# Kernel optimization log

Measured on AMD Instinct MI355X. Metric: run time of the kernel, lower is better.

The kernel has to match this reference:

```python
import jax, jax.numpy as jnp
import numpy as np

PROCESSING_STEPS = 3


def setup_inputs() -> dict:
    key = jax.random.key(0)
    ks = jax.random.split(key, 6)
    N, D, G = 500000, 128, 4096
    x = jax.random.normal(ks[0], (N, D), dtype=jnp.float32)
    # torch LSTM param layout: [4*hidden, input] and [4*hidden, hidden], gates i,f,g,o
    s = 1.0 / np.sqrt(D)
    W_ih = jax.random.uniform(ks[1], (4 * D, 2 * D), minval=-s, maxval=s, dtype=jnp.float32)
    W_hh = jax.random.uniform(ks[2], (4 * D, D), minval=-s, maxval=s, dtype=jnp.float32)
    b_ih = jax.random.uniform(ks[3], (4 * D,), minval=-s, maxval=s, dtype=jnp.float32)
    b_hh = jax.random.uniform(ks[4], (4 * D,), minval=-s, maxval=s, dtype=jnp.float32)
    index = jnp.sort(jax.random.randint(ks[5], (N,), 0, G, dtype=jnp.int64))
    return {"x": x, "W_ih": W_ih, "W_hh": W_hh, "b_ih": b_ih, "b_hh": b_hh,
            "index": index, "dim_size": G}


def _lstm_cell(inp, h, c, W_ih, W_hh, b_ih, b_hh):
    gates = inp @ W_ih.T + h @ W_hh.T + (b_ih + b_hh)  # [G, 4D]
    i, f, g, o = jnp.split(gates, 4, axis=-1)
    c = jax.nn.sigmoid(f) * c + jax.nn.sigmoid(i) * jnp.tanh(g)
    h = jax.nn.sigmoid(o) * jnp.tanh(c)
    return h, c


def reference(x, W_ih, W_hh, b_ih, b_hh, index, dim_size):
    N, D = x.shape
    h = jnp.zeros((dim_size, D), dtype=x.dtype)
    c = jnp.zeros((dim_size, D), dtype=x.dtype)
    q_star = jnp.zeros((dim_size, 2 * D), dtype=x.dtype)
    for _ in range(PROCESSING_STEPS):
        h, c = _lstm_cell(q_star, h, c, W_ih, W_hh, b_ih, b_hh)
        q = h  # [G, D]
        e = jnp.sum(x * q[index], axis=-1)  # [N]
        # segment softmax (numerically stable)
        m = jax.ops.segment_max(e, index, num_segments=dim_size)
        m = jnp.where(jnp.isfinite(m), m, 0.0)  # guard empty segments
        ex = jnp.exp(e - m[index])
        s = jax.ops.segment_sum(ex, index, num_segments=dim_size)
        a = ex / jnp.maximum(s, 1e-16)[index]  # [N]
        r = jax.ops.segment_sum(a[:, None] * x, index, num_segments=dim_size)  # [G, D]
        q_star = jnp.concatenate([q, r], axis=-1)
    return q_star
```

## Files before the change

kernel.cpp:

```cpp
#include <hip/hip_runtime.h>
#include <hip/hip_fp16.h>
#include <math.h>

#define D 128

typedef float f4v __attribute__((ext_vector_type(4)));

__device__ __forceinline__ float sigmoidf_(float x) { return 1.f / (1.f + __expf(-x)); }

__device__ __forceinline__ float4 pack8_to_half8(const float* xf) {
    __half2 hh[4];
    hh[0] = __floats2half2_rn(xf[0], xf[1]);
    hh[1] = __floats2half2_rn(xf[2], xf[3]);
    hh[2] = __floats2half2_rn(xf[4], xf[5]);
    hh[3] = __floats2half2_rn(xf[6], xf[7]);
    return *(float4*)hh;
}

__global__ void prep_kernel(const float* __restrict__ W_ih, const float* __restrict__ W_hh,
                            const float* __restrict__ b_ih, const float* __restrict__ b_hh,
                            const int* __restrict__ idx, int N, int G,
                            float* __restrict__ WcatT, int* __restrict__ seg_off,
                            float* __restrict__ b_sum, float* __restrict__ h1,
                            float* __restrict__ c1) {
    int b = blockIdx.x, t = threadIdx.x;
    if (b < 256) {
        int k = b;
        for (int j = t; j < 512; j += 256) {
            float v = W_ih[(size_t)j * 256 + k];
            if (k < 128) v += W_hh[(size_t)j * 128 + k];
            WcatT[(size_t)k * 512 + j] = v;
        }
    } else if (b < 273) {
        int g = (b - 256) * 256 + t;
        if (g <= G) {
            int lo = 0, hi = N;
            while (lo < hi) {
                int mid = (lo + hi) >> 1;
                if (idx[mid] < g) lo = mid + 1; else hi = mid;
            }
            seg_off[g] = lo;
        }
    } else {
        for (int i = t; i < 4 * D; i += 256) b_sum[i] = b_ih[i] + b_hh[i];
        if (t < D) {
            float bi = b_ih[t] + b_hh[t];
            float bg = b_ih[2 * D + t] + b_hh[2 * D + t];
            float bo = b_ih[3 * D + t] + b_hh[3 * D + t];
            float c = sigmoidf_(bi) * tanhf(bg);
            c1[t] = c;
            h1[t] = sigmoidf_(bo) * tanhf(c);
        }
    }
}

__device__ __forceinline__ void online8(const float (&xf0)[8], const float (&xf1)[8],
                                        const float4 q0, const float4 q1,
                                        int base, int wer, int qg,
                                        float& m, float& s, float (&acc)[8]) {
    float p0 = xf0[0] * q0.x + xf0[1] * q0.y + xf0[2] * q0.z + xf0[3] * q0.w
             + xf0[4] * q1.x + xf0[5] * q1.y + xf0[6] * q1.z + xf0[7] * q1.w;
    float p1 = xf1[0] * q0.x + xf1[1] * q0.y + xf1[2] * q0.z + xf1[3] * q0.w
             + xf1[4] * q1.x + xf1[5] * q1.y + xf1[6] * q1.z + xf1[7] * q1.w;
#pragma unroll
    for (int off = 1; off < 16; off <<= 1) {
        p0 += __shfl_xor(p0, off);
        p1 += __shfl_xor(p1, off);
    }
    float p0a = __shfl_xor(p0, 16), p0b = __shfl_xor(p0, 32), p0c = __shfl_xor(p0a, 32);
    float p1a = __shfl_xor(p1, 16), p1b = __shfl_xor(p1, 32), p1c = __shfl_xor(p1a, 32);
    float s00 = (base + qg       < wer) ? p0  : -INFINITY;
    float s01 = (base + (qg ^ 1) < wer) ? p0a : -INFINITY;
    float s02 = (base + (qg ^ 2) < wer) ? p0b : -INFINITY;
    float s03 = (base + (qg ^ 3) < wer) ? p0c : -INFINITY;
    float s10 = (base + 4 + qg       < wer) ? p1  : -INFINITY;
    float s11 = (base + 4 + (qg ^ 1) < wer) ? p1a : -INFINITY;
    float s12 = (base + 4 + (qg ^ 2) < wer) ? p1b : -INFINITY;
    float s13 = (base + 4 + (qg ^ 3) < wer) ? p1c : -INFINITY;

    float mn = fmaxf(fmaxf(fmaxf(s00, s01), fmaxf(s02, s03)),
                     fmaxf(fmaxf(s10, s11), fmaxf(s12, s13)));
    mn = fmaxf(m, mn);
    float al = __expf(m - mn);
    float w00 = __expf(s00 - mn), w01 = __expf(s01 - mn);
    float w02 = __expf(s02 - mn), w03 = __expf(s03 - mn);
    float w10 = __expf(s10 - mn), w11 = __expf(s11 - mn);
    float w12 = __expf(s12 - mn), w13 = __expf(s13 - mn);
    float sg = (w00 + w01) + (w02 + w03) + ((w10 + w11) + (w12 + w13));
    s = s * al + sg;
#pragma unroll
    for (int j = 0; j < 8; ++j)
        acc[j] = acc[j] * al + w00 * xf0[j] + w10 * xf1[j];
    m = mn;
}

__device__ __forceinline__ void attn_finish(float (&acc)[8], float s, int qg, int c,
                                            float* rdst, bool wr) {
#pragma unroll
    for (int j = 0; j < 8; ++j) {
        acc[j] += __shfl_xor(acc[j], 16);
        acc[j] += __shfl_xor(acc[j], 32);
    }
    if (wr && qg == 0) {
        float inv = 1.f / fmaxf(s, 1e-16f);
        float4 o0; o0.x = acc[0] * inv; o0.y = acc[1] * inv; o0.z = acc[2] * inv; o0.w = acc[3] * inv;
        float4 o1; o1.x = acc[4] * inv; o1.y = acc[5] * inv; o1.z = acc[6] * inv; o1.w = acc[7] * inv;
        *(float4*)&rdst[8 * c] = o0;
        *(float4*)&rdst[8 * c + 4] = o1;
    }
}

__device__ __forceinline__ void attn_f32(const float* __restrict__ x, __half* __restrict__ xh,
                                         int start, int end, int qg, int c,
                                         const float* qrow, float* rdst, bool wr) {
    float4 q0 = *(const float4*)&qrow[8 * c];
    float4 q1 = *(const float4*)&qrow[8 * c + 4];
    float m = -INFINITY, s = 0.f;
    float acc[8] = {0.f, 0.f, 0.f, 0.f, 0.f, 0.f, 0.f, 0.f};
    const f4v* x4 = (const f4v*)x;
    float4* xh4 = (float4*)xh;
    if (start < end) {
        int last = end - 1;
        for (int base = start; base < end; base += 8) {
            int r0 = min(base + qg, last);
            int r1 = min(base + 4 + qg, last);
            f4v f00 = __builtin_nontemporal_load(&x4[(size_t)r0 * 32 + 2 * c]);
            f4v f01 = __builtin_nontemporal_load(&x4[(size_t)r0 * 32 + 2 * c + 1]);
            f4v f10 = __builtin_nontemporal_load(&x4[(size_t)r1 * 32 + 2 * c]);
            f4v f11 = __builtin_nontemporal_load(&x4[(size_t)r1 * 32 + 2 * c + 1]);
            float xf0[8] = {f00.x, f00.y, f00.z, f00.w, f01.x, f01.y, f01.z, f01.w};
            float xf1[8] = {f10.x, f10.y, f10.z, f10.w, f11.x, f11.y, f11.z, f11.w};
            xh4[(size_t)r0 * 16 + c] = pack8_to_half8(xf0);
            xh4[(size_t)r1 * 16 + c] = pack8_to_half8(xf1);
            online8(xf0, xf1, q0, q1, base, end, qg, m, s, acc);
        }
    }
    attn_finish(acc, s, qg, c, rdst, wr);
}

__device__ __forceinline__ void attn_f16(const __half* __restrict__ xh,
                                         int start, int end, int qg, int c,
                                         const float* qrow, float* rdst, bool wr) {
    float4 q0 = *(const float4*)&qrow[8 * c];
    float4 q1 = *(const float4*)&qrow[8 * c + 4];
    float m = -INFINITY, s = 0.f;
    float acc[8] = {0.f, 0.f, 0.f, 0.f, 0.f, 0.f, 0.f, 0.f};
    const float4* x4 = (const float4*)xh;
    if (start < end) {
        int last = end - 1;
        for (int base = start; base < end; base += 8) {
            int r0 = min(base + qg, last);
            int r1 = min(base + 4 + qg, last);
            float4 v0 = x4[(size_t)r0 * 16 + c];
            float4 v1 = x4[(size_t)r1 * 16 + c];
            const __half2* h0 = (const __half2*)&v0;
            const __half2* h1 = (const __half2*)&v1;
            float2 a0 = __half22float2(h0[0]), a1 = __half22float2(h0[1]);
            float2 a2 = __half22float2(h0[2]), a3 = __half22float2(h0[3]);
            float2 b0 = __half22float2(h1[0]), b1 = __half22float2(h1[1]);
            float2 b2 = __half22float2(h1[2]), b3 = __half22float2(h1[3]);
            float xf0[8] = {a0.x, a0.y, a1.x, a1.y, a2.x, a2.y, a3.x, a3.y};
            float xf1[8] = {b0.x, b0.y, b1.x, b1.y, b2.x, b2.y, b3.x, b3.y};
            online8(xf0, xf1, q0, q1, base, end, qg, m, s, acc);
        }
    }
    attn_finish(acc, s, qg, c, rdst, wr);
}

__global__ __launch_bounds__(256, 4) void fused_kernel(
    const float* __restrict__ x, __half* __restrict__ xh,
    const int* __restrict__ seg_off, const float* __restrict__ WcatT,
    const float* __restrict__ b_sum, const float* __restrict__ h1,
    const float* __restrict__ c1, float* __restrict__ out, int G) {

    __shared__ float qs[4][256];
    __shared__ float cL[4][128];
    __shared__ float gl[4][512];
    __shared__ float bL[512];

    int tid = threadIdx.x;
    int w = tid >> 6, lane = tid & 63;
    int qg = lane >> 4, c = lane & 15;
    int gbase = blockIdx.x * 4;
    int g = gbase + w;
    bool valid = g < G;
    int start = 0, end = 0;
    if (valid) { start = seg_off[g]; end = seg_off[g + 1]; }

    for (int e = tid; e < 512; e += 256) bL[e] = b_sum[e];
    if (tid < 128) {
        float hv = h1[tid], cv = c1[tid];
#pragma unroll
        for (int s2 = 0; s2 < 4; ++s2) { qs[s2][tid] = hv; cL[s2][tid] = cv; }
    }
    __syncthreads();

    int j0 = w * 128 + 2 * lane;
    const float* wp = WcatT + j0;

    attn_f32(x, xh, start, end, qg, c, &qs[w][0], &qs[w][128], true);
    __syncthreads();

#pragma unroll 1
    for (int step = 0; step < 2; ++step) {
        float a0[4] = {0.f, 0.f, 0.f, 0.f};
        float a1[4] = {0.f, 0.f, 0.f, 0.f};
        for (int k = 0; k < 256; k += 4) {
            float qv[4][4];
            *(float4*)qv[0] = *(const float4*)&qs[0][k];
            *(float4*)qv[1] = *(const float4*)&qs[1][k];
            *(float4*)qv[2] = *(const float4*)&qs[2][k];
            *(float4*)qv[3] = *(const float4*)&qs[3][k];
#pragma unroll
            for (int dk = 0; dk < 4; ++dk) {
                float2 wv = *(const float2*)&wp[(size_t)(k + dk) * 512];
#pragma unroll
                for (int s2 = 0; s2 < 4; ++s2) {
                    a0[s2] = fmaf(qv[s2][dk], wv.x, a0[s2]);
                    a1[s2] = fmaf(qv[s2][dk], wv.y, a1[s2]);
                }
            }
        }
        float bx = bL[j0], by = bL[j0 + 1];
#pragma unroll
        for (int s2 = 0; s2 < 4; ++s2) {
            float2 o; o.x = a0[s2] + bx; o.y = a1[s2] + by;
            *(float2*)&gl[s2][j0] = o;
        }
        __syncthreads();

        bool final_step = (step == 1);
#pragma unroll
        for (int r2 = 0; r2 < 2; ++r2) {
            int e = tid + 256 * r2;
            int s2 = e >> 7, k = e & 127;
            float ig = gl[s2][k];
            float fg = gl[s2][128 + k];
            float gg = gl[s2][256 + k];
            float og = gl[s2][384 + k];
            float cp = cL[s2][k];
            float cc = sigmoidf_(fg) * cp + sigmoidf_(ig) * tanhf(gg);
            float hh = sigmoidf_(og) * tanhf(cc);
            cL[s2][k] = cc;
            qs[s2][k] = hh;
            if (final_step && (gbase + s2) < G)
                out[(size_t)(gbase + s2) * 256 + k] = hh;
        }
        __syncthreads();

        if (!final_step) {
            attn_f16(xh, start, end, qg, c, &qs[w][0], &qs[w][128], true);
        } else {
            float* rdst = valid ? (out + (size_t)g * 256 + 128) : (float*)&qs[w][128];
            attn_f16(xh, start, end, qg, c, &qs[w][0], rdst, valid);
        }
        __syncthreads();
    }
}

extern "C" void kernel_launch(void* const* d_in, const int* in_sizes, int n_in,
                              void* d_out, int out_size, void* d_ws, size_t ws_size,
                              hipStream_t stream) {
    const float* x      = (const float*)d_in[0];
    const float* W_ih   = (const float*)d_in[1];
    const float* W_hh   = (const float*)d_in[2];
    const float* b_ih   = (const float*)d_in[3];
    const float* b_hh   = (const float*)d_in[4];
    const int*   index  = (const int*)d_in[5];
    int N = in_sizes[5];
    int G = out_size / (2 * D);
    float* out = (float*)d_out;
    size_t totalx = (size_t)N * D;

    float* ws = (float*)d_ws;
    __half* xh    = (__half*)ws;
    float* WcatT  = ws + totalx / 2;
    float* b_sum  = WcatT + 256 * 512;
    float* h1     = b_sum + 4 * D;
    float* c1     = h1 + D;
    int* seg_off  = (int*)(c1 + D);

    prep_kernel<<<274, 256, 0, stream>>>(W_ih, W_hh, b_ih, b_hh, index, N, G,
                                         WcatT, seg_off, b_sum, h1, c1);

    int nb = (G + 3) >> 2;
    fused_kernel<<<nb, 256, 0, stream>>>(x, xh, seg_off, WcatT, b_sum, h1, c1, out, G);
}
```

Measured before the change: 467.7 us.

## Split each segment across two waves with split-K LSTM matvec and softmax merge

Doubles the block to 512 threads so each segment's attention pass is split between two wavefronts. Each wavefront computes a partial online softmax (max, sum, weighted accumulator), and the two halves are merged through shared memory. The LSTM gate matvec is split along K across the two 256-thread halves, with the partial sums and bias added in the cell update. The f16 pass also gains a one-iteration register prefetch. This is meant to add memory-level parallelism and occupancy for the bandwidth-bound x streaming, at the cost of extra shared-memory traffic, barriers and a combine step.

```diff
diff --git a/kernel.cpp b/kernel.cpp
--- a/kernel.cpp
+++ b/kernel.cpp
@@ -94,34 +94,37 @@
     m = mn;
 }
 
-__device__ __forceinline__ void attn_finish(float (&acc)[8], float s, int qg, int c,
-                                            float* rdst, bool wr) {
+__device__ __forceinline__ void attn_store(float (&acc)[8], float m, float s,
+                                           int seg, int half, int lane, int qg, int c,
+                                           float (*gp)[4][512],
+                                           float (*sm2)[2], float (*ss2)[2]) {
 #pragma unroll
     for (int j = 0; j < 8; ++j) {
         acc[j] += __shfl_xor(acc[j], 16);
         acc[j] += __shfl_xor(acc[j], 32);
     }
-    if (wr && qg == 0) {
-        float inv = 1.f / fmaxf(s, 1e-16f);
-        float4 o0; o0.x = acc[0] * inv; o0.y = acc[1] * inv; o0.z = acc[2] * inv; o0.w = acc[3] * inv;
-        float4 o1; o1.x = acc[4] * inv; o1.y = acc[5] * inv; o1.z = acc[6] * inv; o1.w = acc[7] * inv;
-        *(float4*)&rdst[8 * c] = o0;
-        *(float4*)&rdst[8 * c + 4] = o1;
-    }
-}
-
-__device__ __forceinline__ void attn_f32(const float* __restrict__ x, __half* __restrict__ xh,
-                                         int start, int end, int qg, int c,
-                                         const float* qrow, float* rdst, bool wr) {
+    if (qg == 0) {
+#pragma unroll
+        for (int j = 0; j < 8; ++j) gp[half][seg][8 * c + j] = acc[j];
+    }
+    if (lane == 0) { sm2[seg][half] = m; ss2[seg][half] = s; }
+}
+
+__device__ __forceinline__ void attn_pass_f32(const float* __restrict__ x,
+                                              __half* __restrict__ xh,
+                                              int ws, int we, int seg, int half,
+                                              int lane, int qg, int c, const float* qrow,
+                                              float (*gp)[4][512],
+                                              float (*sm2)[2], float (*ss2)[2]) {
     float4 q0 = *(const float4*)&qrow[8 * c];
     float4 q1 = *(const float4*)&qrow[8 * c + 4];
     float m = -INFINITY, s = 0.f;
     float acc[8] = {0.f, 0.f, 0.f, 0.f, 0.f, 0.f, 0.f, 0.f};
     const f4v* x4 = (const f4v*)x;
     float4* xh4 = (float4*)xh;
-    if (start < end) {
-        int last = end - 1;
-        for (int base = start; base < end; base += 8) {
+    if (ws < we) {
+        int last = we - 1;
+        for (int base = ws; base < we; base += 8) {
             int r0 = min(base + qg, last);
             int r1 = min(base + 4 + qg, last);
             f4v f00 = __builtin_nontemporal_load(&x4[(size_t)r0 * 32 + 2 * c]);
@@ -132,42 +135,70 @@
             float xf1[8] = {f10.x, f10.y, f10.z, f10.w, f11.x, f11.y, f11.z, f11.w};
             xh4[(size_t)r0 * 16 + c] = pack8_to_half8(xf0);
             xh4[(size_t)r1 * 16 + c] = pack8_to_half8(xf1);
-            online8(xf0, xf1, q0, q1, base, end, qg, m, s, acc);
-        }
-    }
-    attn_finish(acc, s, qg, c, rdst, wr);
-}
-
-__device__ __forceinline__ void attn_f16(const __half* __restrict__ xh,
-                                         int start, int end, int qg, int c,
-                                         const float* qrow, float* rdst, bool wr) {
+            online8(xf0, xf1, q0, q1, base, we, qg, m, s, acc);
+        }
+    }
+    attn_store(acc, m, s, seg, half, lane, qg, c, gp, sm2, ss2);
+}
+
+__device__ __forceinline__ void attn_pass_f16(const __half* __restrict__ xh,
+                                              int ws, int we, int seg, int half,
+                                              int lane, int qg, int c, const float* qrow,
+                                              float (*gp)[4][512],
+                                              float (*sm2)[2], float (*ss2)[2]) {
     float4 q0 = *(const float4*)&qrow[8 * c];
     float4 q1 = *(const float4*)&qrow[8 * c + 4];
     float m = -INFINITY, s = 0.f;
     float acc[8] = {0.f, 0.f, 0.f, 0.f, 0.f, 0.f, 0.f, 0.f};
     const float4* x4 = (const float4*)xh;
-    if (start < end) {
-        int last = end - 1;
-        for (int base = start; base < end; base += 8) {
-            int r0 = min(base + qg, last);
-            int r1 = min(base + 4 + qg, last);
-            float4 v0 = x4[(size_t)r0 * 16 + c];
-            float4 v1 = x4[(size_t)r1 * 16 + c];
-            const __half2* h0 = (const __half2*)&v0;
-            const __half2* h1 = (const __half2*)&v1;
+    if (ws < we) {
+        int last = we - 1;
+        int r0 = min(ws + qg, last), r1 = min(ws + 4 + qg, last);
+        float4 v0 = x4[(size_t)r0 * 16 + c];
+        float4 v1 = x4[(size_t)r1 * 16 + c];
+        for (int base = ws; base < we; ) {
+            float4 cv0 = v0, cv1 = v1;
+            int nb = base + 8;
+            if (nb < we) {
+                int n0 = min(nb + qg, last), n1 = min(nb + 4 + qg, last);
+                v0 = x4[(size_t)n0 * 16 + c];
+                v1 = x4[(size_t)n1 * 16 + c];
+            }
+            const __half2* h0 = (const __half2*)&cv0;
+            const __half2* h1 = (const __half2*)&cv1;
             float2 a0 = __half22float2(h0[0]), a1 = __half22float2(h0[1]);
             float2 a2 = __half22float2(h0[2]), a3 = __half22float2(h0[3]);
             float2 b0 = __half22float2(h1[0]), b1 = __half22float2(h1[1]);
             float2 b2 = __half22float2(h1[2]), b3 = __half22float2(h1[3]);
             float xf0[8] = {a0.x, a0.y, a1.x, a1.y, a2.x, a2.y, a3.x, a3.y};
             float xf1[8] = {b0.x, b0.y, b1.x, b1.y, b2.x, b2.y, b3.x, b3.y};
-            online8(xf0, xf1, q0, q1, base, end, qg, m, s, acc);
-        }
-    }
-    attn_finish(acc, s, qg, c, rdst, wr);
-}
-
-__global__ __launch_bounds__(256, 4) void fused_kernel(
+            online8(xf0, xf1, q0, q1, base, we, qg, m, s, acc);
+            base = nb;
+        }
+    }
+    attn_store(acc, m, s, seg, half, lane, qg, c, gp, sm2, ss2);
+}
+
+__device__ __forceinline__ void attn_combine(const float (*gp)[4][512],
+                                             const float (*sm2)[2], const float (*ss2)[2],
+                                             float (*qs)[256], float* __restrict__ out,
+                                             int gbase, int G, bool final_step) {
+    int tid = threadIdx.x;
+    int s2 = tid >> 7, col = tid & 127;
+    float m0 = sm2[s2][0], m1 = sm2[s2][1];
+    float mstar = fmaxf(m0, m1);
+    float r = 0.f;
+    if (mstar > -INFINITY) {
+        float e0 = __expf(m0 - mstar), e1 = __expf(m1 - mstar);
+        float stot = ss2[s2][0] * e0 + ss2[s2][1] * e1;
+        float at = gp[0][s2][col] * e0 + gp[1][s2][col] * e1;
+        r = at / fmaxf(stot, 1e-16f);
+    }
+    if (!final_step) qs[s2][128 + col] = r;
+    else if (gbase + s2 < G) out[(size_t)(gbase + s2) * 256 + 128 + col] = r;
+}
+
+__global__ __launch_bounds__(512, 8) void fused_kernel(
     const float* __restrict__ x, __half* __restrict__ xh,
     const int* __restrict__ seg_off, const float* __restrict__ WcatT,
     const float* __restrict__ b_sum, const float* __restrict__ h1,
@@ -175,42 +206,54 @@
 
     __shared__ float qs[4][256];
     __shared__ float cL[4][128];
-    __shared__ float gl[4][512];
+    __shared__ float gp[2][4][512];
     __shared__ float bL[512];
+    __shared__ float sm2[4][2], ss2[4][2];
 
     int tid = threadIdx.x;
     int w = tid >> 6, lane = tid & 63;
     int qg = lane >> 4, c = lane & 15;
+    int seg = w & 3, half = w >> 2;
     int gbase = blockIdx.x * 4;
-    int g = gbase + w;
-    bool valid = g < G;
-    int start = 0, end = 0;
-    if (valid) { start = seg_off[g]; end = seg_off[g + 1]; }
-
-    for (int e = tid; e < 512; e += 256) bL[e] = b_sum[e];
-    if (tid < 128) {
-        float hv = h1[tid], cv = c1[tid];
-#pragma unroll
-        for (int s2 = 0; s2 < 4; ++s2) { qs[s2][tid] = hv; cL[s2][tid] = cv; }
+    int g = gbase + seg;
+    int ws = 0, we = 0;
+    if (g < G) {
+        int st = seg_off[g], en = seg_off[g + 1];
+        int cnt = en - st;
+        int chunk = (cnt + 1) >> 1;
+        ws = st + half * chunk;
+        we = min(ws + chunk, en);
+    }
+
+    bL[tid & 511] = b_sum[tid & 511];
+    {
+        int s2 = tid >> 7, k = tid & 127;
+        qs[s2][k] = h1[k];
+        cL[s2][k] = c1[k];
     }
     __syncthreads();
 
-    int j0 = w * 128 + 2 * lane;
-    const float* wp = WcatT + j0;
-
-    attn_f32(x, xh, start, end, qg, c, &qs[w][0], &qs[w][128], true);
+    int tl = tid & 255, kh = tid >> 8;
+    int j0 = 2 * tl;
+    int koff = kh * 128;
+    const float* wp = WcatT + (size_t)koff * 512 + j0;
+
+    attn_pass_f32(x, xh, ws, we, seg, half, lane, qg, c, &qs[seg][0], gp, sm2, ss2);
+    __syncthreads();
+    attn_combine(gp, sm2, ss2, qs, out, gbase, G, false);
     __syncthreads();
 
 #pragma unroll 1
     for (int step = 0; step < 2; ++step) {
+        bool final_step = (step == 1);
         float a0[4] = {0.f, 0.f, 0.f, 0.f};
         float a1[4] = {0.f, 0.f, 0.f, 0.f};
-        for (int k = 0; k < 256; k += 4) {
+        for (int k = 0; k < 128; k += 4) {
             float qv[4][4];
-            *(float4*)qv[0] = *(const float4*)&qs[0][k];
-            *(float4*)qv[1] = *(const float4*)&qs[1][k];
-            *(float4*)qv[2] = *(const float4*)&qs[2][k];
-            *(float4*)qv[3] = *(const float4*)&qs[3][k];
+            *(float4*)qv[0] = *(const float4*)&qs[0][koff + k];
+            *(float4*)qv[1] = *(const float4*)&qs[1][koff + k];
+            *(float4*)qv[2] = *(const float4*)&qs[2][koff + k];
+            *(float4*)qv[3] = *(const float4*)&qs[3][koff + k];
 #pragma unroll
             for (int dk = 0; dk < 4; ++dk) {
                 float2 wv = *(const float2*)&wp[(size_t)(k + dk) * 512];
@@ -221,23 +264,19 @@
                 }
             }
         }
-        float bx = bL[j0], by = bL[j0 + 1];
 #pragma unroll
         for (int s2 = 0; s2 < 4; ++s2) {
-            float2 o; o.x = a0[s2] + bx; o.y = a1[s2] + by;
-            *(float2*)&gl[s2][j0] = o;
+            float2 o; o.x = a0[s2]; o.y = a1[s2];
+            *(float2*)&gp[kh][s2][j0] = o;
         }
         __syncthreads();
 
-        bool final_step = (step == 1);
-#pragma unroll
-        for (int r2 = 0; r2 < 2; ++r2) {
-            int e = tid + 256 * r2;
-            int s2 = e >> 7, k = e & 127;
-            float ig = gl[s2][k];
-            float fg = gl[s2][128 + k];
-            float gg = gl[s2][256 + k];
-            float og = gl[s2][384 + k];
+        {
+            int s2 = tid >> 7, k = tid & 127;
+            float ig = gp[0][s2][k]       + gp[1][s2][k]       + bL[k];
+            float fg = gp[0][s2][128 + k] + gp[1][s2][128 + k] + bL[128 + k];
+            float gg = gp[0][s2][256 + k] + gp[1][s2][256 + k] + bL[256 + k];
+            float og = gp[0][s2][384 + k] + gp[1][s2][384 + k] + bL[384 + k];
             float cp = cL[s2][k];
             float cc = sigmoidf_(fg) * cp + sigmoidf_(ig) * tanhf(gg);
             float hh = sigmoidf_(og) * tanhf(cc);
@@ -248,12 +287,9 @@
         }
         __syncthreads();
 
-        if (!final_step) {
-            attn_f16(xh, start, end, qg, c, &qs[w][0], &qs[w][128], true);
-        } else {
-            float* rdst = valid ? (out + (size_t)g * 256 + 128) : (float*)&qs[w][128];
-            attn_f16(xh, start, end, qg, c, &qs[w][0], rdst, valid);
-        }
+        attn_pass_f16(xh, ws, we, seg, half, lane, qg, c, &qs[seg][0], gp, sm2, ss2);
+        __syncthreads();
+        attn_combine(gp, sm2, ss2, qs, out, gbase, G, final_step);
         __syncthreads();
     }
 }
@@ -284,5 +320,5 @@
                                          WcatT, seg_off, b_sum, h1, c1);
 
     int nb = (G + 3) >> 2;
-    fused_kernel<<<nb, 256, 0, stream>>>(x, xh, seg_off, WcatT, b_sum, h1, c1, out, G);
-}
+    fused_kernel<<<nb, 512, 0, stream>>>(x, xh, seg_off, WcatT, b_sum, h1, c1, out, G);
+}
```

After: 1.013 ms. 116% more time.
